# Kernel tuning notes

Hardware: AMD Instinct MI355X
Metric: run time of the kernel (lower is better)

Reference implementation:

```python
import jax, jax.numpy as jnp
import numpy as np

BETA = 0.25
N_E = 8192
E_DIM = 256
BATCH = 32768


def setup_inputs() -> dict:
    key = jax.random.key(0)
    kx, kc = jax.random.split(key)
    x = jax.random.normal(kx, (BATCH, E_DIM), dtype=jnp.float32)
    centroids = jax.random.normal(kc, (N_E, E_DIM), dtype=jnp.float32)
    return {"x": x, "centroids": centroids}


def reference(x, centroids):
    x_norm = jnp.sum(x * x, axis=1, keepdims=True)            # [B, 1]
    c_norm = jnp.sum(centroids * centroids, axis=1)           # [n_e]
    distances = x_norm + c_norm[None, :] - 2.0 * (x @ centroids.T)
    indices = jnp.argmin(distances, axis=-1)                  # [B]
    x_q = centroids[indices]                                  # [B, e_dim] gather
    commitment_loss = jnp.mean((jax.lax.stop_gradient(x_q) - x) ** 2)
    codebook_loss = jnp.mean((x_q - jax.lax.stop_gradient(x)) ** 2)
    loss = codebook_loss + BETA * commitment_loss
    # straight-through estimator
    x_q_out = x + jax.lax.stop_gradient(x_q - x)
    return x_q_out, loss, indices
```

## Files before the change

### kernel.cpp

```cpp
#include <hip/hip_runtime.h>
#include <hip/hip_fp16.h>
#include <stdint.h>

#define BATCH 32768
#define NE    8192
#define DIM   256
#define LOSS_OFF 8388608
#define IDX_OFF  8388609
#define MARGIN 0.25f

typedef _Float16 v8h  __attribute__((ext_vector_type(8)));
typedef _Float16 v4h  __attribute__((ext_vector_type(4)));
typedef float    f32x4 __attribute__((ext_vector_type(4)));
typedef unsigned long long ull;

#define GLOAD_LDS16(g, l) __builtin_amdgcn_global_load_lds( \
    (const __attribute__((address_space(1))) void*)(g),     \
    (__attribute__((address_space(3))) void*)(l), 16, 0, 0)


__device__ __forceinline__ unsigned enc_key(float f) {
  unsigned b = __float_as_uint(f);
  return (b & 0x80000000u) ? ~b : (b | 0x80000000u);
}
__device__ __forceinline__ float dec_key(unsigned kb) {
  return __uint_as_float((kb & 0x80000000u) ? (kb ^ 0x80000000u) : ~kb);
}

__global__ __launch_bounds__(256) void vq_prep_x(
    const float* __restrict__ x, _Float16* __restrict__ Ahi,
    float* __restrict__ xn, float* __restrict__ out) {
  const int w = threadIdx.x >> 6, lane = threadIdx.x & 63;
  const int row = blockIdx.x * 4 + w;
  const float4 v = *(const float4*)(x + (size_t)row * DIM + (lane << 2));
  v4h h = { (_Float16)v.x, (_Float16)v.y, (_Float16)v.z, (_Float16)v.w };
  *(v4h*)(Ahi + (size_t)row * DIM + (lane << 2)) = h;
  float s = v.x * v.x + v.y * v.y + v.z * v.z + v.w * v.w;
  #pragma unroll
  for (int off = 32; off > 0; off >>= 1) s += __shfl_down(s, off);
  if (lane == 0) xn[row] = s;
  if (row == 0 && lane == 0) out[LOSS_OFF] = 0.0f;
}

__global__ __launch_bounds__(256) void vq_prep_c(
    const float* __restrict__ c, _Float16* __restrict__ Bhi,
    float* __restrict__ cn) {
  const int w = threadIdx.x >> 6, lane = threadIdx.x & 63;
  const int row = blockIdx.x * 4 + w;
  const float4 v = *(const float4*)(c + (size_t)row * DIM + (lane << 2));
  v4h h = { (_Float16)v.x, (_Float16)v.y, (_Float16)v.z, (_Float16)v.w };
  *(v4h*)(Bhi + (size_t)row * DIM + (lane << 2)) = h;
  float s = v.x * v.x + v.y * v.y + v.z * v.z + v.w * v.w;
  #pragma unroll
  for (int off = 32; off > 0; off >>= 1) s += __shfl_down(s, off);
  if (lane == 0) cn[row] = s;
}

__global__ __launch_bounds__(256) void vq_gemm1(
    const _Float16* __restrict__ A, const _Float16* __restrict__ B,
    const float* __restrict__ cn, ull* __restrict__ cand) {
  __shared__ _Float16 As[2][128 * 64];
  __shared__ _Float16 Bs[2][128 * 64];

  const int tid = threadIdx.x, w = tid >> 6, lane = tid & 63;
  const int nt = blockIdx.x, mt = blockIdx.y;
  const int rowBase = mt * 128, colBase = nt * 128;
  const int l15 = lane & 15, l4 = lane >> 4;
  const int st_row = (w << 3) + (lane >> 3);
  const int st_slot = lane & 7;

  f32x4 acc[2][8];
  #pragma unroll
  for (int mi = 0; mi < 2; ++mi)
    #pragma unroll
    for (int ni = 0; ni < 8; ++ni) acc[mi][ni] = (f32x4)0.0f;

  auto STAGE = [&](int buf, int kc) {
    #pragma unroll
    for (int i = 0; i < 4; ++i) {
      const int r = (i << 5) + st_row;
      const int s = st_slot ^ (r & 7);
      GLOAD_LDS16(A + (size_t)(rowBase + r) * DIM + kc * 64 + s * 8,
                  &As[buf][((i << 5) + (w << 3)) * 64]);
      GLOAD_LDS16(B + (size_t)(colBase + r) * DIM + kc * 64 + s * 8,
                  &Bs[buf][((i << 5) + (w << 3)) * 64]);
    }
  };

  STAGE(0, 0);
  __syncthreads();
  for (int kc = 0; kc < 4; ++kc) {
    const int cur = kc & 1;
    if (kc < 3) STAGE(cur ^ 1, kc + 1);
    #pragma unroll
    for (int ks = 0; ks < 2; ++ks) {
      v8h a[2], b[8];
      #pragma unroll
      for (int mi = 0; mi < 2; ++mi) {
        const int r = (w << 5) + mi * 16 + l15;
        const int slot = ((ks << 2) + l4) ^ (r & 7);
        a[mi] = *(const v8h*)&As[cur][r * 64 + slot * 8];
      }
      #pragma unroll
      for (int ni = 0; ni < 8; ++ni) {
        const int cc = ni * 16 + l15;
        const int slot = ((ks << 2) + l4) ^ (cc & 7);
        b[ni] = *(const v8h*)&Bs[cur][cc * 64 + slot * 8];
      }
      #pragma unroll
      for (int mi = 0; mi < 2; ++mi)
        #pragma unroll
        for (int ni = 0; ni < 8; ++ni)
          acc[mi][ni] = __builtin_amdgcn_mfma_f32_16x16x32_f16(
              a[mi], b[ni], acc[mi][ni], 0, 0, 0);
    }
    __syncthreads();
  }

  #pragma unroll
  for (int mi = 0; mi < 2; ++mi)
    #pragma unroll
    for (int r = 0; r < 4; ++r) {
      ull f = ~0ull, s = ~0ull;
      #pragma unroll
      for (int ni = 0; ni < 8; ++ni) {
        const int col = colBase + ni * 16 + l15;
        const float key = fmaf(-2.0f, acc[mi][ni][r], cn[col]);
        const ull p = ((ull)enc_key(key) << 32) | (unsigned)col;
        if (p < f) { s = f; f = p; } else if (p < s) { s = p; }
      }
      #pragma unroll
      for (int off = 1; off < 16; off <<= 1) {
        const ull of = __shfl_xor(f, off);
        const ull os = __shfl_xor(s, off);
        ull nf, ns;
        if (f <= of) { nf = f;  ns = (of < s ? of : s); }
        else         { nf = of; ns = (f < os ? f : os); }
        f = nf; s = ns;
      }
      if (l15 == ((mi << 2) | r)) {
        const int row = rowBase + (w << 5) + mi * 16 + (l4 << 2) + r;
        ull* dst = cand + ((size_t)row * 64 + nt) * 2;
        dst[0] = f; dst[1] = s;
      }
    }
}

__global__ __launch_bounds__(256) void vq_refine(
    const ull* __restrict__ cand, const float* __restrict__ x,
    const float* __restrict__ c, const float* __restrict__ xn,
    const float* __restrict__ cn, int* __restrict__ bestIdx) {
  const int w = threadIdx.x >> 6, lane = threadIdx.x & 63;
  const int row = blockIdx.x * 4 + w;
  const ull pf = cand[((size_t)row * 64 + lane) * 2];
  const ull ps = cand[((size_t)row * 64 + lane) * 2 + 1];
  ull gb = pf;
  #pragma unroll
  for (int off = 1; off < 64; off <<= 1) { const ull o = __shfl_xor(gb, off); if (o < gb) gb = o; }
  const unsigned thr = enc_key(dec_key((unsigned)(gb >> 32)) + MARGIN);
  const ull m1 = __ballot((unsigned)(pf >> 32) <= thr);
  const ull m2 = __ballot((unsigned)(ps >> 32) <= thr);
  int winner;
  if (__popcll(m1) == 1 && m2 == 0ull) {
    winner = (int)(unsigned)(gb & 0xffffffffull);
  } else {
    const float4 xv = *(const float4*)(x + (size_t)row * DIM + (lane << 2));
    const float xnr = xn[row];
    float bd = 3.4e38f; int bi = 0x7fffffff;
    for (int pass = 0; pass < 2; ++pass) {
      ull m = (pass == 0) ? m1 : m2;
      while (m) {
        const int src = __ffsll((long long)m) - 1; m &= m - 1;
        const ull p = __shfl((pass == 0) ? pf : ps, src);
        const int idx = (int)(unsigned)(p & 0xffffffffull);
        const float4 cv = *(const float4*)(c + (size_t)idx * DIM + (lane << 2));
        float dsum = xv.x * cv.x + xv.y * cv.y + xv.z * cv.z + xv.w * cv.w;
        #pragma unroll
        for (int off = 1; off < 64; off <<= 1) dsum += __shfl_xor(dsum, off);
        const float d = xnr + cn[idx] - 2.0f * dsum;
        if (d < bd || (d == bd && idx < bi)) { bd = d; bi = idx; }
      }
    }
    winner = bi;
  }
  if (lane == 0) bestIdx[row] = winner;
}

__global__ __launch_bounds__(256) void vq_finish(
    const float* __restrict__ x, const float* __restrict__ c,
    const int* __restrict__ bestIdx, float* __restrict__ out) {
  __shared__ float red[4];
  const int w = threadIdx.x >> 6, lane = threadIdx.x & 63;
  float s = 0.0f;
  #pragma unroll 4
  for (int i = 0; i < 32; ++i) {
    const int row = blockIdx.x * 128 + i * 4 + w;
    const int idx = bestIdx[row];
    const float4 q = *(const float4*)(c + (size_t)idx * DIM + (lane << 2));
    const float4 v = *(const float4*)(x + (size_t)row * DIM + (lane << 2));
    *(float4*)(out + (size_t)row * DIM + (lane << 2)) = q;
    const float dx = q.x - v.x, dy = q.y - v.y, dz = q.z - v.z, dw = q.w - v.w;
    s += dx * dx + dy * dy + dz * dz + dw * dw;
    if (lane == 0) out[IDX_OFF + row] = (float)idx;
  }
  #pragma unroll
  for (int off = 32; off > 0; off >>= 1) s += __shfl_down(s, off);
  if (lane == 0) red[w] = s;
  __syncthreads();
  if (threadIdx.x == 0) {
    const float t = red[0] + red[1] + red[2] + red[3];
    atomicAdd(&out[LOSS_OFF], t * (1.25f / 8388608.0f));
  }
}

extern "C" void kernel_launch(void* const* d_in, const int* in_sizes, int n_in,
                              void* d_out, int out_size, void* d_ws, size_t ws_size,
                              hipStream_t stream) {
  const float* x = (const float*)d_in[0];
  const float* c = (const float*)d_in[1];
  float* out = (float*)d_out;
  char* ws = (char*)d_ws;
  _Float16* Ahi = (_Float16*)ws;
  _Float16* Bhi = (_Float16*)(ws + 16777216);
  float*    cn  = (float*)(ws + 20971520);
  float*    xn  = (float*)(ws + 21004288);
  int*  bestIdx = (int*)(ws + 21135360);
  ull*     cand = (ull*)(ws + 21266432);

  vq_prep_x<<<BATCH / 4, 256, 0, stream>>>(x, Ahi, xn, out);
  vq_prep_c<<<NE / 4,    256, 0, stream>>>(c, Bhi, cn);
  dim3 grid(NE / 128, BATCH / 128, 1);
  vq_gemm1 <<<grid, 256, 0, stream>>>(Ahi, Bhi, cn, cand);
  vq_refine<<<BATCH / 4, 256, 0, stream>>>(cand, x, c, xn, cn, bestIdx);
  vq_finish<<<BATCH / 128, 256, 0, stream>>>(x, c, bestIdx, out);
}
```

Measured before the change: 459.7 us.

## Fuse full-codebook sweep with per-lane top-3 packed keys in GEMM

The GEMM kernel is restructured so each block owns 128 rows and keeps its A fragments in registers for the whole K. It streams all 64 codebook tiles through a double-buffered LDS and keeps a running top-3 per lane, using 32-bit keys that pack the biased distance bits with the tile and subtile index. This replaces the 64x256 grid, which wrote two 64-bit candidates per row per column tile. That cuts candidate traffic and shrinks the refine kernel's reduction. The risks are that the launch has only 256 blocks at one block per CU with 128 KB of LDS, so occupancy drops, and that truncating the mantissa with the wider margin may send more rows down the slow exact path.

```diff
diff --git a/kernel.cpp b/kernel.cpp
--- a/kernel.cpp
+++ b/kernel.cpp
@@ -7,7 +7,8 @@
 #define DIM   256
 #define LOSS_OFF 8388608
 #define IDX_OFF  8388609
-#define MARGIN 0.25f
+#define KBIAS  768.0f
+#define MARGIN 0.5f
 
 typedef _Float16 v8h  __attribute__((ext_vector_type(8)));
 typedef _Float16 v4h  __attribute__((ext_vector_type(4)));
@@ -18,14 +19,6 @@
     (const __attribute__((address_space(1))) void*)(g),     \
     (__attribute__((address_space(3))) void*)(l), 16, 0, 0)
 
-
-__device__ __forceinline__ unsigned enc_key(float f) {
-  unsigned b = __float_as_uint(f);
-  return (b & 0x80000000u) ? ~b : (b | 0x80000000u);
-}
-__device__ __forceinline__ float dec_key(unsigned kb) {
-  return __uint_as_float((kb & 0x80000000u) ? (kb ^ 0x80000000u) : ~kb);
-}
 
 __global__ __launch_bounds__(256) void vq_prep_x(
     const float* __restrict__ x, _Float16* __restrict__ Ahi,
@@ -56,130 +49,136 @@
   if (lane == 0) cn[row] = s;
 }
 
-__global__ __launch_bounds__(256) void vq_gemm1(
+__global__ __launch_bounds__(256, 1) void vq_gemm_topk(
     const _Float16* __restrict__ A, const _Float16* __restrict__ B,
-    const float* __restrict__ cn, ull* __restrict__ cand) {
-  __shared__ _Float16 As[2][128 * 64];
-  __shared__ _Float16 Bs[2][128 * 64];
+    const float* __restrict__ cn, unsigned* __restrict__ cand) {
+  __shared__ _Float16 Bs[2][128 * 256];
 
   const int tid = threadIdx.x, w = tid >> 6, lane = tid & 63;
-  const int nt = blockIdx.x, mt = blockIdx.y;
-  const int rowBase = mt * 128, colBase = nt * 128;
   const int l15 = lane & 15, l4 = lane >> 4;
-  const int st_row = (w << 3) + (lane >> 3);
-  const int st_slot = lane & 7;
-
-  f32x4 acc[2][8];
+  const int rowBase = blockIdx.x * 128;
+  const int wrow = w << 5;
+
+  v8h a[2][8];
   #pragma unroll
   for (int mi = 0; mi < 2; ++mi)
     #pragma unroll
-    for (int ni = 0; ni < 8; ++ni) acc[mi][ni] = (f32x4)0.0f;
-
-  auto STAGE = [&](int buf, int kc) {
-    #pragma unroll
-    for (int i = 0; i < 4; ++i) {
-      const int r = (i << 5) + st_row;
-      const int s = st_slot ^ (r & 7);
-      GLOAD_LDS16(A + (size_t)(rowBase + r) * DIM + kc * 64 + s * 8,
-                  &As[buf][((i << 5) + (w << 3)) * 64]);
-      GLOAD_LDS16(B + (size_t)(colBase + r) * DIM + kc * 64 + s * 8,
-                  &Bs[buf][((i << 5) + (w << 3)) * 64]);
-    }
+    for (int ks = 0; ks < 8; ++ks)
+      a[mi][ks] = *(const v8h*)(A + (size_t)(rowBase + wrow + mi * 16 + l15) * DIM
+                                  + ks * 32 + l4 * 8);
+
+  unsigned k0[2][4], k1[2][4], k2[2][4];
+  #pragma unroll
+  for (int mi = 0; mi < 2; ++mi)
+    #pragma unroll
+    for (int r = 0; r < 4; ++r) { k0[mi][r] = k1[mi][r] = k2[mi][r] = 0xFFFFFFFFu; }
+
+  auto STAGE = [&](int buf, int tile) {
+    const _Float16* src = B + ((size_t)tile * 128 + lane) * DIM + w * 64;
+    #pragma unroll
+    for (int j = 0; j < 16; ++j)
+      GLOAD_LDS16(src + (j & 1) * 16384 + (j >> 1) * 8,
+                  &Bs[buf][(w * 16 + j) * 512]);
   };
 
   STAGE(0, 0);
-  __syncthreads();
-  for (int kc = 0; kc < 4; ++kc) {
-    const int cur = kc & 1;
-    if (kc < 3) STAGE(cur ^ 1, kc + 1);
-    #pragma unroll
-    for (int ks = 0; ks < 2; ++ks) {
-      v8h a[2], b[8];
-      #pragma unroll
-      for (int mi = 0; mi < 2; ++mi) {
-        const int r = (w << 5) + mi * 16 + l15;
-        const int slot = ((ks << 2) + l4) ^ (r & 7);
-        a[mi] = *(const v8h*)&As[cur][r * 64 + slot * 8];
-      }
-      #pragma unroll
-      for (int ni = 0; ni < 8; ++ni) {
-        const int cc = ni * 16 + l15;
-        const int slot = ((ks << 2) + l4) ^ (cc & 7);
-        b[ni] = *(const v8h*)&Bs[cur][cc * 64 + slot * 8];
-      }
+  const int ldb = l4 * 1024 + l15 * 8;
+
+  #pragma unroll 1
+  for (int t = 0; t < 64; ++t) {
+    __syncthreads();
+    const int cur = t & 1;
+    STAGE(cur ^ 1, (t + 1) & 63);
+
+    float cnb[8];
+    #pragma unroll
+    for (int ni = 0; ni < 8; ++ni)
+      cnb[ni] = cn[t * 128 + ni * 16 + l15] + KBIAS;
+
+    f32x4 acc[2][8];
+    #pragma unroll
+    for (int mi = 0; mi < 2; ++mi)
+      #pragma unroll
+      for (int ni = 0; ni < 8; ++ni) acc[mi][ni] = (f32x4)0.0f;
+
+    #pragma unroll
+    for (int ks = 0; ks < 8; ++ks) {
+      v8h b[8];
+      #pragma unroll
+      for (int ni = 0; ni < 8; ++ni)
+        b[ni] = *(const v8h*)&Bs[cur][ks * 4096 + ldb + ni * 128];
       #pragma unroll
       for (int mi = 0; mi < 2; ++mi)
         #pragma unroll
         for (int ni = 0; ni < 8; ++ni)
           acc[mi][ni] = __builtin_amdgcn_mfma_f32_16x16x32_f16(
-              a[mi], b[ni], acc[mi][ni], 0, 0, 0);
+              a[mi][ks], b[ni], acc[mi][ni], 0, 0, 0);
     }
-    __syncthreads();
+
+    #pragma unroll
+    for (int mi = 0; mi < 2; ++mi)
+      #pragma unroll
+      for (int ni = 0; ni < 8; ++ni)
+        #pragma unroll
+        for (int r = 0; r < 4; ++r) {
+          const float d = fmaf(-2.0f, acc[mi][ni][r], cnb[ni]);
+          const unsigned p = (__float_as_uint(d) & 0xFFFFFE00u)
+                           | (unsigned)((t << 3) | ni);
+          const bool b2 = p < k2[mi][r];
+          const bool b1 = p < k1[mi][r];
+          const bool b0 = p < k0[mi][r];
+          k2[mi][r] = b2 ? (b1 ? k1[mi][r] : p) : k2[mi][r];
+          k1[mi][r] = b1 ? (b0 ? k0[mi][r] : p) : k1[mi][r];
+          k0[mi][r] = b0 ? p : k0[mi][r];
+        }
   }
 
   #pragma unroll
   for (int mi = 0; mi < 2; ++mi)
     #pragma unroll
     for (int r = 0; r < 4; ++r) {
-      ull f = ~0ull, s = ~0ull;
-      #pragma unroll
-      for (int ni = 0; ni < 8; ++ni) {
-        const int col = colBase + ni * 16 + l15;
-        const float key = fmaf(-2.0f, acc[mi][ni][r], cn[col]);
-        const ull p = ((ull)enc_key(key) << 32) | (unsigned)col;
-        if (p < f) { s = f; f = p; } else if (p < s) { s = p; }
-      }
-      #pragma unroll
-      for (int off = 1; off < 16; off <<= 1) {
-        const ull of = __shfl_xor(f, off);
-        const ull os = __shfl_xor(s, off);
-        ull nf, ns;
-        if (f <= of) { nf = f;  ns = (of < s ? of : s); }
-        else         { nf = of; ns = (f < os ? f : os); }
-        f = nf; s = ns;
-      }
-      if (l15 == ((mi << 2) | r)) {
-        const int row = rowBase + (w << 5) + mi * 16 + (l4 << 2) + r;
-        ull* dst = cand + ((size_t)row * 64 + nt) * 2;
-        dst[0] = f; dst[1] = s;
-      }
+      const size_t row = rowBase + wrow + mi * 16 + l4 * 4 + r;
+      cand[row * 48 +      l15] = k0[mi][r];
+      cand[row * 48 + 16 + l15] = k1[mi][r];
+      cand[row * 48 + 32 + l15] = k2[mi][r];
     }
 }
 
 __global__ __launch_bounds__(256) void vq_refine(
-    const ull* __restrict__ cand, const float* __restrict__ x,
+    const unsigned* __restrict__ cand, const float* __restrict__ x,
     const float* __restrict__ c, const float* __restrict__ xn,
     const float* __restrict__ cn, int* __restrict__ bestIdx) {
   const int w = threadIdx.x >> 6, lane = threadIdx.x & 63;
   const int row = blockIdx.x * 4 + w;
-  const ull pf = cand[((size_t)row * 64 + lane) * 2];
-  const ull ps = cand[((size_t)row * 64 + lane) * 2 + 1];
-  ull gb = pf;
-  #pragma unroll
-  for (int off = 1; off < 64; off <<= 1) { const ull o = __shfl_xor(gb, off); if (o < gb) gb = o; }
-  const unsigned thr = enc_key(dec_key((unsigned)(gb >> 32)) + MARGIN);
-  const ull m1 = __ballot((unsigned)(pf >> 32) <= thr);
-  const ull m2 = __ballot((unsigned)(ps >> 32) <= thr);
+  const unsigned p = (lane < 48) ? cand[(size_t)row * 48 + lane] : 0xFFFFFFFFu;
+  unsigned mn = p;
+  #pragma unroll
+  for (int off = 1; off < 64; off <<= 1) {
+    const unsigned o = __shfl_xor(mn, off);
+    if (o < mn) mn = o;
+  }
+  const float thr = __uint_as_float(mn & 0xFFFFFE00u) + MARGIN;
+  const bool inm = (lane < 48) && (__uint_as_float(p & 0xFFFFFE00u) <= thr);
+  const ull m = __ballot(inm);
   int winner;
-  if (__popcll(m1) == 1 && m2 == 0ull) {
-    winner = (int)(unsigned)(gb & 0xffffffffull);
+  if (__popcll(m) == 1) {
+    const int src = __ffsll((long long)m) - 1;
+    winner = (int)(((mn >> 3) & 63) * 128 + (mn & 7) * 16 + (src & 15));
   } else {
     const float4 xv = *(const float4*)(x + (size_t)row * DIM + (lane << 2));
     const float xnr = xn[row];
     float bd = 3.4e38f; int bi = 0x7fffffff;
-    for (int pass = 0; pass < 2; ++pass) {
-      ull m = (pass == 0) ? m1 : m2;
-      while (m) {
-        const int src = __ffsll((long long)m) - 1; m &= m - 1;
-        const ull p = __shfl((pass == 0) ? pf : ps, src);
-        const int idx = (int)(unsigned)(p & 0xffffffffull);
-        const float4 cv = *(const float4*)(c + (size_t)idx * DIM + (lane << 2));
-        float dsum = xv.x * cv.x + xv.y * cv.y + xv.z * cv.z + xv.w * cv.w;
-        #pragma unroll
-        for (int off = 1; off < 64; off <<= 1) dsum += __shfl_xor(dsum, off);
-        const float d = xnr + cn[idx] - 2.0f * dsum;
-        if (d < bd || (d == bd && idx < bi)) { bd = d; bi = idx; }
-      }
+    ull mm = m;
+    while (mm) {
+      const int src = __ffsll((long long)mm) - 1; mm &= mm - 1;
+      const unsigned pw = __shfl(p, src);
+      const int idx = (int)(((pw >> 3) & 63) * 128 + (pw & 7) * 16 + (src & 15));
+      const float4 cv = *(const float4*)(c + (size_t)idx * DIM + (lane << 2));
+      float dsum = xv.x * cv.x + xv.y * cv.y + xv.z * cv.z + xv.w * cv.w;
+      #pragma unroll
+      for (int off = 1; off < 64; off <<= 1) dsum += __shfl_xor(dsum, off);
+      const float d = xnr + cn[idx] - 2.0f * dsum;
+      if (d < bd || (d == bd && idx < bi)) { bd = d; bi = idx; }
     }
     winner = bi;
   }
@@ -225,12 +224,11 @@
   float*    cn  = (float*)(ws + 20971520);
   float*    xn  = (float*)(ws + 21004288);
   int*  bestIdx = (int*)(ws + 21135360);
-  ull*     cand = (ull*)(ws + 21266432);
+  unsigned* cand = (unsigned*)(ws + 21266432);
 
   vq_prep_x<<<BATCH / 4, 256, 0, stream>>>(x, Ahi, xn, out);
   vq_prep_c<<<NE / 4,    256, 0, stream>>>(c, Bhi, cn);
-  dim3 grid(NE / 128, BATCH / 128, 1);
-  vq_gemm1 <<<grid, 256, 0, stream>>>(Ahi, Bhi, cn, cand);
+  vq_gemm_topk<<<256,    256, 0, stream>>>(Ahi, Bhi, cn, cand);
   vq_refine<<<BATCH / 4, 256, 0, stream>>>(cand, x, c, xn, cn, bestIdx);
   vq_finish<<<BATCH / 128, 256, 0, stream>>>(x, c, bestIdx, out);
 }
```

After: 483.5 us. +5.2%, slower.
